# Kernel tuning notes

Hardware: AMD Instinct MI355X
Metric: run time of the kernel (lower is better)

Reference implementation:

```python
import jax, jax.numpy as jnp
import numpy as np

B, S, D, H, DH = 4, 1024, 1024, 16, 64  # batch, seq, d_model, heads, head dim (d_Q=d_K=d_V)


def setup_inputs() -> dict:
    key = jax.random.key(0)
    ks = jax.random.split(key, 12)
    std = 0.02
    return {
        "x_Q": jax.random.normal(ks[0], (B, S, D), jnp.float32),
        "x_K": jax.random.normal(ks[1], (B, S, D), jnp.float32),
        "x_V": jax.random.normal(ks[2], (B, S, D), jnp.float32),
        "src_batch_lens": jax.random.randint(ks[3], (B,), 0, S),
        # stacked per-head projection weights: [H, d_model, head_dim]
        "Wq": jax.random.normal(ks[4], (H, D, DH), jnp.float32) * std,
        "bq": jax.random.normal(ks[5], (H, DH), jnp.float32) * std,
        "Wk": jax.random.normal(ks[6], (H, D, DH), jnp.float32) * std,
        "bk": jax.random.normal(ks[7], (H, DH), jnp.float32) * std,
        "Wv": jax.random.normal(ks[8], (H, D, DH), jnp.float32) * std,
        "bv": jax.random.normal(ks[9], (H, DH), jnp.float32) * std,
        "Wo": jax.random.normal(ks[10], (D, D), jnp.float32) * std,
        "bo": jax.random.normal(ks[11], (D,), jnp.float32) * std,
    }


def reference(x_Q, x_K, x_V, src_batch_lens, Wq, bq, Wk, bk, Wv, bv, Wo, bo):
    dq = Wq.shape[-1]
    seq = x_Q.shape[1]
    # all heads at once instead of the per-head python loop
    Q = jnp.einsum('bsd,hde->bhse', x_Q, Wq) + bq[None, :, None, :]
    K = jnp.einsum('bsd,hde->bhse', x_K, Wk) + bk[None, :, None, :]
    V = jnp.einsum('bsd,hde->bhse', x_V, Wv) + bv[None, :, None, :]
    scores = jnp.einsum('bhse,bhte->bhst', Q, K) / jnp.sqrt(jnp.asarray(dq, x_Q.dtype))
    # original: matmul(diag(1..1,0..0), scores) zeroes query rows >= length
    rowmask = (jnp.arange(seq)[None, :] < src_batch_lens[:, None])  # [B, S]
    scores = scores * rowmask[:, None, :, None].astype(scores.dtype)
    A = jax.nn.softmax(scores, axis=-1)  # torch Softmax(dim=2) on [B,S,S] per head = key axis
    AV = jnp.einsum('bhst,bhtv->bhsv', A, V)
    out = AV.transpose(0, 2, 1, 3).reshape(x_Q.shape[0], seq, -1)  # concat heads on dim 2
    return out @ Wo + bo  # dropout p=0 -> identity
```

## Files before the change

### kernel.cpp

```cpp
#include <hip/hip_runtime.h>
#include <stdint.h>

typedef short v8s __attribute__((ext_vector_type(8)));
typedef short v4s __attribute__((ext_vector_type(4)));
typedef float v4f __attribute__((ext_vector_type(4)));

#define AS1 __attribute__((address_space(1)))
#define AS3 __attribute__((address_space(3)))

__device__ __forceinline__ void glds16(const void* g, void* l) {
  __builtin_amdgcn_global_load_lds((const AS1 void*)g, (AS3 void*)l, 16, 0, 0);
}

__device__ __forceinline__ short f2bf(float f) {
  uint32_t u = __float_as_uint(f);
  u += 0x7fffu + ((u >> 16) & 1u);
  return (short)(u >> 16);
}


__global__ __launch_bounds__(256) void cast3_f32_bf16(
    const float* __restrict__ a, const float* __restrict__ b, const float* __restrict__ c,
    short* __restrict__ oa, short* __restrict__ ob, short* __restrict__ oc, int n4) {
  const float* in = (blockIdx.z == 0) ? a : (blockIdx.z == 1) ? b : c;
  short* out      = (blockIdx.z == 0) ? oa : (blockIdx.z == 1) ? ob : oc;
  int i = blockIdx.x * 256 + threadIdx.x;
  if (i < n4) {
    float4 v = ((const float4*)in)[i];
    short4 o = { f2bf(v.x), f2bf(v.y), f2bf(v.z), f2bf(v.w) };
    ((short4*)out)[i] = o;
  }
}

__global__ __launch_bounds__(256) void transpose_w_all(
    const float* __restrict__ wq, const float* __restrict__ wk, const float* __restrict__ wv,
    const float* __restrict__ wo,
    short* __restrict__ oq, short* __restrict__ ok, short* __restrict__ ov,
    short* __restrict__ oo) {
  __shared__ float tile[64][65];
  const int z = blockIdx.z;
  const float* in;
  short* out;
  int C, R, rb, cb;
  if (z < 3) {
    const int slice = blockIdx.y;
    in  = ((z == 0) ? wq : (z == 1) ? wk : wv) + (size_t)slice * 65536;
    out = ((z == 0) ? oq : (z == 1) ? ok : ov) + (size_t)slice * 65536;
    C = 64; R = 1024; rb = blockIdx.x * 64; cb = 0;
  } else {
    in = wo; out = oo;
    C = 1024; R = 1024; rb = blockIdx.x * 64; cb = blockIdx.y * 64;
  }
  int t = threadIdx.x;
  int col = t & 63, r0 = t >> 6;
#pragma unroll
  for (int i = 0; i < 16; ++i) {
    int row = r0 + i * 4;
    tile[row][col] = in[(size_t)(rb + row) * C + cb + col];
  }
  __syncthreads();
#pragma unroll
  for (int i = 0; i < 16; ++i) {
    int orow = r0 + i * 4;
    out[(size_t)(cb + orow) * R + rb + col] = f2bf(tile[col][orow]);
  }
}

template <int MR>
__device__ __forceinline__ void gemm_core(const short* __restrict__ Ag,
                                          const short* __restrict__ Bg,
                                          short* As, short* Bs,
                                          v4f (&acc)[MR / 32][4]) {
  constexpr int MT = MR / 32;
  constexpr int ASZ = MR * 32;
  constexpr int BSZ = 128 * 32;
  const int tid  = threadIdx.x;
  const int lane = tid & 63;
  const int w    = tid >> 6;
  const int quad = lane >> 4;
  const int c15  = lane & 15;
  const int wr   = (w >> 1) * (MR / 2);
  const int wc   = (w & 1) * 64;

  const int r0 = tid >> 2, p0 = tid & 3;
  const short* a0 = Ag + (size_t)r0 * 1024 + p0 * 8;
  const short* a1 = a0 + 64 * 1024;
  const short* b0 = Bg + (size_t)r0 * 1024 + p0 * 8;
  const short* b1 = b0 + 64 * 1024;
  short* lA = As + tid * 8;
  short* lB = Bs + tid * 8;

  auto issue = [&](int t, int buf) {
    const int o = t * 32;
    glds16(a0 + o, lA + buf * ASZ);
    if constexpr (MR == 128) glds16(a1 + o, lA + buf * ASZ + 2048);
    glds16(b0 + o, lB + buf * BSZ);
    glds16(b1 + o, lB + buf * BSZ + 2048);
  };

  issue(0, 0);
  issue(1, 1);

  for (int kb = 0; kb < 32; ++kb) {
    if constexpr (MR == 128)
      asm volatile("s_waitcnt vmcnt(4)\n\ts_barrier" ::: "memory");
    else
      asm volatile("s_waitcnt vmcnt(3)\n\ts_barrier" ::: "memory");

    const int t2 = kb + 2;
    issue(t2 < 32 ? t2 : 31, t2 % 3);

    const short* Ab = As + (kb % 3) * ASZ;
    const short* Bb = Bs + (kb % 3) * BSZ;

    v8s a[MT], b[4];
#pragma unroll
    for (int mt = 0; mt < MT; ++mt)
      a[mt] = *(const v8s*)(Ab + (wr + mt * 16 + c15) * 32 + quad * 8);
#pragma unroll
    for (int nt = 0; nt < 4; ++nt)
      b[nt] = *(const v8s*)(Bb + (wc + nt * 16 + c15) * 32 + quad * 8);
#pragma unroll
    for (int mt = 0; mt < MT; ++mt)
#pragma unroll
      for (int nt = 0; nt < 4; ++nt)
        acc[mt][nt] = __builtin_amdgcn_mfma_f32_16x16x32_bf16(a[mt], b[nt], acc[mt][nt], 0, 0, 0);
  }
}

__global__ __launch_bounds__(256, 3) void proj_gemm(
    const short* __restrict__ xQ, const short* __restrict__ xK, const short* __restrict__ xV,
    const short* __restrict__ WqT, const short* __restrict__ WkT, const short* __restrict__ WvT,
    const float* __restrict__ bq, const float* __restrict__ bk, const float* __restrict__ bv,
    short* __restrict__ Qb, short* __restrict__ Kb, short* __restrict__ Vtb) {
  __shared__ short As[12288];
  __shared__ short Bs[12288];
  const int lin = blockIdx.x;
  const int z = lin >> 8;
  const int r = lin & 255;
  const int nb = ((r >> 3) & 7) * 128;
  const int mb = (((r & 7) << 2) + (r >> 6)) * 128;
  const short* A    = (z == 0) ? xQ  : (z == 1) ? xK  : xV;
  const short* Bt   = (z == 0) ? WqT : (z == 1) ? WkT : WvT;
  const float* bias = (z == 0) ? bq  : (z == 1) ? bk  : bv;
  short* outp       = (z == 0) ? Qb  : (z == 1) ? Kb  : Vtb;
  v4f acc[4][4] = {};
  gemm_core<128>(A + (size_t)mb * 1024, Bt + (size_t)nb * 1024, As, Bs, acc);

  const int lane = threadIdx.x & 63, w = threadIdx.x >> 6;
  const int quad = lane >> 4, c15 = lane & 15;
  const int wr = (w >> 1) * 64, wc = (w & 1) * 64;
  const bool vmode = (z == 2);
#pragma unroll
  for (int nt = 0; nt < 4; ++nt) {
    const int gn = nb + wc + nt * 16 + c15;
    const float bb = bias[gn];
    const int h = gn >> 6, e = gn & 63;
#pragma unroll
    for (int mt = 0; mt < 4; ++mt) {
      if (!vmode) {
#pragma unroll
        for (int rr = 0; rr < 4; ++rr) {
          const int gm = mb + wr + mt * 16 + quad * 4 + rr;
          const int bi = gm >> 10, s = gm & 1023;
          const size_t base = (size_t)(bi * 16 + h) * 65536;
          outp[base + (size_t)s * 64 + e] = f2bf(acc[mt][nt][rr] + bb);
        }
      } else {
        const int gm0 = mb + wr + mt * 16 + quad * 4;
        const int bi = gm0 >> 10, s0 = gm0 & 1023;
        const size_t base = (size_t)(bi * 16 + h) * 65536;
        short4 st = { f2bf(acc[mt][nt][0] + bb), f2bf(acc[mt][nt][1] + bb),
                      f2bf(acc[mt][nt][2] + bb), f2bf(acc[mt][nt][3] + bb) };
        *(short4*)&outp[base + (size_t)e * 1024 + s0] = st;
      }
    }
  }
}

__global__ __launch_bounds__(256, 3) void out_gemm(
    const short* __restrict__ AV, const short* __restrict__ WoT,
    const float* __restrict__ bo, float* __restrict__ outp) {
  __shared__ short As[6144];
  __shared__ short Bs[12288];
  const int lin = blockIdx.x;
  const int nb = ((lin >> 3) & 7) * 128;
  const int mb = (((lin & 7) << 3) + (lin >> 6)) * 64;
  v4f acc[2][4] = {};
  gemm_core<64>(AV + (size_t)mb * 1024, WoT + (size_t)nb * 1024, As, Bs, acc);
  const int lane = threadIdx.x & 63, w = threadIdx.x >> 6;
  const int quad = lane >> 4, c15 = lane & 15;
  const int wr = (w >> 1) * 32, wc = (w & 1) * 64;
#pragma unroll
  for (int nt = 0; nt < 4; ++nt) {
    const int gn = nb + wc + nt * 16 + c15;
    const float bb = bo[gn];
#pragma unroll
    for (int mt = 0; mt < 2; ++mt)
#pragma unroll
      for (int r = 0; r < 4; ++r) {
        const int gm = mb + wr + mt * 16 + quad * 4 + r;
        outp[(size_t)gm * 1024 + gn] = acc[mt][nt][r] + bb;
      }
  }
}

__global__ __launch_bounds__(256, 2) void attn_kernel(
    const short* __restrict__ Qb, const short* __restrict__ Kb,
    const short* __restrict__ Vtb, const int* __restrict__ lens,
    short* __restrict__ AVb) {
  __shared__ short Ks[2][4096];
  __shared__ short Vs[2][4096];
  const int tid = threadIdx.x, lane = tid & 63, w = tid >> 6;
  const int quad = lane >> 4, c15 = lane & 15;
  const int flat = blockIdx.x;
  const int bh = (flat & 7) + 8 * ((flat >> 3) & 7);
  const int qg = flat >> 6;
  const int b = bh >> 4, h = bh & 15;
  const short* Qp = Qb  + (size_t)bh * 65536;
  const short* Kp = Kb  + (size_t)bh * 65536;
  const short* Vp = Vtb + (size_t)bh * 65536;
  const int len = lens[b];
  const int row0 = qg * 128 + w * 32;

  v8s bq_[2][2];
#pragma unroll
  for (int mg = 0; mg < 2; ++mg)
#pragma unroll
    for (int kf = 0; kf < 2; ++kf)
      bq_[mg][kf] = *(const v8s*)(Qp + (size_t)(row0 + mg * 16 + c15) * 64 + kf * 32 + quad * 8);

  float scale[2];
#pragma unroll
  for (int mg = 0; mg < 2; ++mg)
    scale[mg] = (row0 + mg * 16 + c15 < len) ? 0.125f : 0.0f;

  float sm[2] = { 0.f, 0.f };
  v4f o[2][4] = {};

  const int srow = tid >> 3, spart = tid & 7;
  const int gpart = spart ^ (srow & 7);
  const int kgo0 = srow * 64 + gpart * 8, kgo1 = (srow + 32) * 64 + gpart * 8;
  const int vgo0 = srow * 1024 + gpart * 8, vgo1 = (srow + 32) * 1024 + gpart * 8;
  const int l0 = tid * 8, l1 = 2048 + tid * 8;

  const int c7 = c15 & 7;
  const int krow = c15 * 128;
  const int koff0 = krow + ((quad) ^ c7) * 16;
  const int koff1 = krow + ((4 + quad) ^ c7) * 16;
  const int q2 = quad >> 1, h8 = (quad & 1) * 8;
  int voff[4];
#pragma unroll
  for (int nt = 0; nt < 4; ++nt)
    voff[nt] = krow + ((2 * nt + q2) ^ c7) * 16 + h8;

  glds16(Kp + kgo0, (char*)Ks[0] + l0 * 2);
  glds16(Kp + kgo1, (char*)Ks[0] + l1 * 2);
  glds16(Vp + vgo0, (char*)Vs[0] + l0 * 2);
  glds16(Vp + vgo1, (char*)Vs[0] + l1 * 2);

  for (int kb = 0; kb < 16; ++kb) {
    const int cur = kb & 1, nxt = cur ^ 1;
    __syncthreads();

    if (kb < 15) {
      const short* kt = Kp + (size_t)(kb + 1) * 4096;
      const short* vt = Vp + (kb + 1) * 64;
      glds16(kt + kgo0, (char*)Ks[nxt] + l0 * 2);
      glds16(kt + kgo1, (char*)Ks[nxt] + l1 * 2);
      glds16(vt + vgo0, (char*)Vs[nxt] + l0 * 2);
      glds16(vt + vgo1, (char*)Vs[nxt] + l1 * 2);
    }

    v8s ak[4][2];
#pragma unroll
    for (int nt = 0; nt < 4; ++nt) {
      ak[nt][0] = *(const v8s*)((const char*)Ks[cur] + nt * 2048 + koff0);
      ak[nt][1] = *(const v8s*)((const char*)Ks[cur] + nt * 2048 + koff1);
    }
    v4s av[4][4];
#pragma unroll
    for (int t = 0; t < 4; ++t)
#pragma unroll
      for (int nt = 0; nt < 4; ++nt)
        av[t][nt] = *(const v4s*)((const char*)Vs[cur] + t * 2048 + voff[nt]);

    v4f sc[2][4];
#pragma unroll
    for (int mg = 0; mg < 2; ++mg)
#pragma unroll
      for (int nt = 0; nt < 4; ++nt) {
        v4f z = {};
#pragma unroll
        for (int kf = 0; kf < 2; ++kf)
          z = __builtin_amdgcn_mfma_f32_16x16x32_bf16(ak[nt][kf], bq_[mg][kf], z, 0, 0, 0);
        sc[mg][nt] = z;
      }

    v4s pb[2][4];
#pragma unroll
    for (int mg = 0; mg < 2; ++mg)
#pragma unroll
      for (int nt = 0; nt < 4; ++nt) {
        v4s pv;
#pragma unroll
        for (int r = 0; r < 4; ++r) {
          float p = __expf(sc[mg][nt][r] * scale[mg]);
          sm[mg] += p;
          pv[r] = f2bf(p);
        }
        pb[mg][nt] = pv;
      }

#pragma unroll
    for (int mg = 0; mg < 2; ++mg)
#pragma unroll
      for (int t = 0; t < 4; ++t)
#pragma unroll
        for (int nt = 0; nt < 4; ++nt)
          o[mg][t] = __builtin_amdgcn_mfma_f32_16x16x16bf16_1k(av[t][nt], pb[mg][nt], o[mg][t], 0, 0, 0);
  }

#pragma unroll
  for (int mg = 0; mg < 2; ++mg) {
    sm[mg] += __shfl_xor(sm[mg], 16);
    sm[mg] += __shfl_xor(sm[mg], 32);
  }

#pragma unroll
  for (int mg = 0; mg < 2; ++mg) {
    const float inv = 1.0f / sm[mg];
    const size_t rowbase = (size_t)(b * 1024 + row0 + mg * 16 + c15) * 1024 + h * 64;
#pragma unroll
    for (int t = 0; t < 4; ++t) {
      short4 st = { f2bf(o[mg][t][0] * inv), f2bf(o[mg][t][1] * inv),
                    f2bf(o[mg][t][2] * inv), f2bf(o[mg][t][3] * inv) };
      *(short4*)&AVb[rowbase + t * 16 + quad * 4] = st;
    }
  }
}

extern "C" void kernel_launch(void* const* d_in, const int* in_sizes, int n_in,
                              void* d_out, int out_size, void* d_ws, size_t ws_size,
                              hipStream_t stream) {
  const float* xQ = (const float*)d_in[0];
  const float* xK = (const float*)d_in[1];
  const float* xV = (const float*)d_in[2];
  const int* lens = (const int*)d_in[3];
  const float* Wq = (const float*)d_in[4];
  const float* bq = (const float*)d_in[5];
  const float* Wk = (const float*)d_in[6];
  const float* bk = (const float*)d_in[7];
  const float* Wv = (const float*)d_in[8];
  const float* bv = (const float*)d_in[9];
  const float* Wo = (const float*)d_in[10];
  const float* bo = (const float*)d_in[11];
  float* out = (float*)d_out;

  char* ws = (char*)d_ws;
  short* xQb = (short*)(ws + 0);
  short* xKb = (short*)(ws + 8388608);
  short* xVb = (short*)(ws + 16777216);
  short* WqT = (short*)(ws + 25165824);
  short* WkT = (short*)(ws + 27262976);
  short* WvT = (short*)(ws + 29360128);
  short* WoT = (short*)(ws + 31457280);
  short* Qb  = (short*)(ws + 33554432);
  short* Kb  = (short*)(ws + 41943040);
  short* Vtb = (short*)(ws + 50331648);
  short* AVb = (short*)(ws + 58720256);

  cast3_f32_bf16<<<dim3(4096, 1, 3), 256, 0, stream>>>(xQ, xK, xV, xQb, xKb, xVb, 1048576);
  transpose_w_all<<<dim3(16, 16, 4), 256, 0, stream>>>(Wq, Wk, Wv, Wo, WqT, WkT, WvT, WoT);
  proj_gemm<<<dim3(768), 256, 0, stream>>>(xQb, xKb, xVb, WqT, WkT, WvT,
                                           bq, bk, bv, Qb, Kb, Vtb);
  attn_kernel<<<dim3(512), 256, 0, stream>>>(Qb, Kb, Vtb, lens, AVb);
  out_gemm<<<dim3(512), 256, 0, stream>>>(AVb, WoT, bo, out);
}
```

Measured before the change: 204.9 us.

## Swizzle GEMM LDS tiles and split attention across 8 waves per block

The GEMM core now XOR-swizzles the 16-byte chunk position within each LDS row, on both the global-to-LDS writes and the fragment reads, to cut LDS bank conflicts. The attention kernel moves to 512 threads per block, with each wave handling 16 query rows instead of 32. Each thread then issues one K and one V async load per tile instead of two. The aim is fewer registers per wave and more waves in flight to hide latency, at the cost of less Q-tile reuse of each K/V fragment read from LDS per wave.

```diff
diff --git a/kernel.cpp b/kernel.cpp
--- a/kernel.cpp
+++ b/kernel.cpp
@@ -82,7 +82,8 @@
   const int wr   = (w >> 1) * (MR / 2);
   const int wc   = (w & 1) * 64;
 
-  const int r0 = tid >> 2, p0 = tid & 3;
+  const int r0 = tid >> 2;
+  const int p0 = (tid & 3) ^ ((r0 & 3) ^ ((r0 >> 2) & 3));
   const short* a0 = Ag + (size_t)r0 * 1024 + p0 * 8;
   const short* a1 = a0 + 64 * 1024;
   const short* b0 = Bg + (size_t)r0 * 1024 + p0 * 8;
@@ -101,6 +102,9 @@
   issue(0, 0);
   issue(1, 1);
 
+  const int xs = (c15 & 3) ^ ((c15 >> 2) & 3);
+  const int rdoff = ((quad ^ xs)) * 8;
+
   for (int kb = 0; kb < 32; ++kb) {
     if constexpr (MR == 128)
       asm volatile("s_waitcnt vmcnt(4)\n\ts_barrier" ::: "memory");
@@ -116,10 +120,10 @@
     v8s a[MT], b[4];
 #pragma unroll
     for (int mt = 0; mt < MT; ++mt)
-      a[mt] = *(const v8s*)(Ab + (wr + mt * 16 + c15) * 32 + quad * 8);
+      a[mt] = *(const v8s*)(Ab + (wr + mt * 16 + c15) * 32 + rdoff);
 #pragma unroll
     for (int nt = 0; nt < 4; ++nt)
-      b[nt] = *(const v8s*)(Bb + (wc + nt * 16 + c15) * 32 + quad * 8);
+      b[nt] = *(const v8s*)(Bb + (wc + nt * 16 + c15) * 32 + rdoff);
 #pragma unroll
     for (int mt = 0; mt < MT; ++mt)
 #pragma unroll
@@ -205,7 +209,7 @@
   }
 }
 
-__global__ __launch_bounds__(256, 2) void attn_kernel(
+__global__ __launch_bounds__(512, 4) void attn_kernel(
     const short* __restrict__ Qb, const short* __restrict__ Kb,
     const short* __restrict__ Vtb, const int* __restrict__ lens,
     short* __restrict__ AVb) {
@@ -221,28 +225,22 @@
   const short* Kp = Kb  + (size_t)bh * 65536;
   const short* Vp = Vtb + (size_t)bh * 65536;
   const int len = lens[b];
-  const int row0 = qg * 128 + w * 32;
-
-  v8s bq_[2][2];
-#pragma unroll
-  for (int mg = 0; mg < 2; ++mg)
-#pragma unroll
-    for (int kf = 0; kf < 2; ++kf)
-      bq_[mg][kf] = *(const v8s*)(Qp + (size_t)(row0 + mg * 16 + c15) * 64 + kf * 32 + quad * 8);
-
-  float scale[2];
-#pragma unroll
-  for (int mg = 0; mg < 2; ++mg)
-    scale[mg] = (row0 + mg * 16 + c15 < len) ? 0.125f : 0.0f;
-
-  float sm[2] = { 0.f, 0.f };
-  v4f o[2][4] = {};
+  const int row0 = qg * 128 + w * 16;
+
+  v8s bq_[2];
+#pragma unroll
+  for (int kf = 0; kf < 2; ++kf)
+    bq_[kf] = *(const v8s*)(Qp + (size_t)(row0 + c15) * 64 + kf * 32 + quad * 8);
+
+  const float scale = (row0 + c15 < len) ? 0.125f : 0.0f;
+  float sm = 0.f;
+  v4f o[4] = {};
 
   const int srow = tid >> 3, spart = tid & 7;
   const int gpart = spart ^ (srow & 7);
-  const int kgo0 = srow * 64 + gpart * 8, kgo1 = (srow + 32) * 64 + gpart * 8;
-  const int vgo0 = srow * 1024 + gpart * 8, vgo1 = (srow + 32) * 1024 + gpart * 8;
-  const int l0 = tid * 8, l1 = 2048 + tid * 8;
+  const int kgo = srow * 64 + gpart * 8;
+  const int vgo = srow * 1024 + gpart * 8;
+  const int l0 = tid * 8;
 
   const int c7 = c15 & 7;
   const int krow = c15 * 128;
@@ -254,22 +252,16 @@
   for (int nt = 0; nt < 4; ++nt)
     voff[nt] = krow + ((2 * nt + q2) ^ c7) * 16 + h8;
 
-  glds16(Kp + kgo0, (char*)Ks[0] + l0 * 2);
-  glds16(Kp + kgo1, (char*)Ks[0] + l1 * 2);
-  glds16(Vp + vgo0, (char*)Vs[0] + l0 * 2);
-  glds16(Vp + vgo1, (char*)Vs[0] + l1 * 2);
+  glds16(Kp + kgo, (char*)Ks[0] + l0 * 2);
+  glds16(Vp + vgo, (char*)Vs[0] + l0 * 2);
 
   for (int kb = 0; kb < 16; ++kb) {
     const int cur = kb & 1, nxt = cur ^ 1;
     __syncthreads();
 
     if (kb < 15) {
-      const short* kt = Kp + (size_t)(kb + 1) * 4096;
-      const short* vt = Vp + (kb + 1) * 64;
-      glds16(kt + kgo0, (char*)Ks[nxt] + l0 * 2);
-      glds16(kt + kgo1, (char*)Ks[nxt] + l1 * 2);
-      glds16(vt + vgo0, (char*)Vs[nxt] + l0 * 2);
-      glds16(vt + vgo1, (char*)Vs[nxt] + l1 * 2);
+      glds16(Kp + (size_t)(kb + 1) * 4096 + kgo, (char*)Ks[nxt] + l0 * 2);
+      glds16(Vp + (kb + 1) * 64 + vgo, (char*)Vs[nxt] + l0 * 2);
     }
 
     v8s ak[4][2];
@@ -278,6 +270,30 @@
       ak[nt][0] = *(const v8s*)((const char*)Ks[cur] + nt * 2048 + koff0);
       ak[nt][1] = *(const v8s*)((const char*)Ks[cur] + nt * 2048 + koff1);
     }
+
+    v4f sc[4];
+#pragma unroll
+    for (int nt = 0; nt < 4; ++nt) {
+      v4f z = {};
+#pragma unroll
+      for (int kf = 0; kf < 2; ++kf)
+        z = __builtin_amdgcn_mfma_f32_16x16x32_bf16(ak[nt][kf], bq_[kf], z, 0, 0, 0);
+      sc[nt] = z;
+    }
+
+    v4s pb[4];
+#pragma unroll
+    for (int nt = 0; nt < 4; ++nt) {
+      v4s pv;
+#pragma unroll
+      for (int r = 0; r < 4; ++r) {
+        float p = __expf(sc[nt][r] * scale);
+        sm += p;
+        pv[r] = f2bf(p);
+      }
+      pb[nt] = pv;
+    }
+
     v4s av[4][4];
 #pragma unroll
     for (int t = 0; t < 4; ++t)
@@ -285,58 +301,23 @@
       for (int nt = 0; nt < 4; ++nt)
         av[t][nt] = *(const v4s*)((const char*)Vs[cur] + t * 2048 + voff[nt]);
 
-    v4f sc[2][4];
-#pragma unroll
-    for (int mg = 0; mg < 2; ++mg)
-#pragma unroll
-      for (int nt = 0; nt < 4; ++nt) {
-        v4f z = {};
-#pragma unroll
-        for (int kf = 0; kf < 2; ++kf)
-          z = __builtin_amdgcn_mfma_f32_16x16x32_bf16(ak[nt][kf], bq_[mg][kf], z, 0, 0, 0);
-        sc[mg][nt] = z;
-      }
-
-    v4s pb[2][4];
-#pragma unroll
-    for (int mg = 0; mg < 2; ++mg)
-#pragma unroll
-      for (int nt = 0; nt < 4; ++nt) {
-        v4s pv;
-#pragma unroll
-        for (int r = 0; r < 4; ++r) {
-          float p = __expf(sc[mg][nt][r] * scale[mg]);
-          sm[mg] += p;
-          pv[r] = f2bf(p);
-        }
-        pb[mg][nt] = pv;
-      }
-
-#pragma unroll
-    for (int mg = 0; mg < 2; ++mg)
-#pragma unroll
-      for (int t = 0; t < 4; ++t)
-#pragma unroll
-        for (int nt = 0; nt < 4; ++nt)
-          o[mg][t] = __builtin_amdgcn_mfma_f32_16x16x16bf16_1k(av[t][nt], pb[mg][nt], o[mg][t], 0, 0, 0);
-  }
-
-#pragma unroll
-  for (int mg = 0; mg < 2; ++mg) {
-    sm[mg] += __shfl_xor(sm[mg], 16);
-    sm[mg] += __shfl_xor(sm[mg], 32);
-  }
-
-#pragma unroll
-  for (int mg = 0; mg < 2; ++mg) {
-    const float inv = 1.0f / sm[mg];
-    const size_t rowbase = (size_t)(b * 1024 + row0 + mg * 16 + c15) * 1024 + h * 64;
-#pragma unroll
-    for (int t = 0; t < 4; ++t) {
-      short4 st = { f2bf(o[mg][t][0] * inv), f2bf(o[mg][t][1] * inv),
-                    f2bf(o[mg][t][2] * inv), f2bf(o[mg][t][3] * inv) };
-      *(short4*)&AVb[rowbase + t * 16 + quad * 4] = st;
-    }
+#pragma unroll
+    for (int t = 0; t < 4; ++t)
+#pragma unroll
+      for (int nt = 0; nt < 4; ++nt)
+        o[t] = __builtin_amdgcn_mfma_f32_16x16x16bf16_1k(av[t][nt], pb[nt], o[t], 0, 0, 0);
+  }
+
+  sm += __shfl_xor(sm, 16);
+  sm += __shfl_xor(sm, 32);
+
+  const float inv = 1.0f / sm;
+  const size_t rowbase = (size_t)(b * 1024 + row0 + c15) * 1024 + h * 64;
+#pragma unroll
+  for (int t = 0; t < 4; ++t) {
+    short4 st = { f2bf(o[t][0] * inv), f2bf(o[t][1] * inv),
+                  f2bf(o[t][2] * inv), f2bf(o[t][3] * inv) };
+    *(short4*)&AVb[rowbase + t * 16 + quad * 4] = st;
   }
 }
 
@@ -374,6 +355,6 @@
   transpose_w_all<<<dim3(16, 16, 4), 256, 0, stream>>>(Wq, Wk, Wv, Wo, WqT, WkT, WvT, WoT);
   proj_gemm<<<dim3(768), 256, 0, stream>>>(xQb, xKb, xVb, WqT, WkT, WvT,
                                            bq, bk, bv, Qb, Kb, Vtb);
-  attn_kernel<<<dim3(512), 256, 0, stream>>>(Qb, Kb, Vtb, lens, AVb);
+  attn_kernel<<<dim3(512), 512, 0, stream>>>(Qb, Kb, Vtb, lens, AVb);
   out_gemm<<<dim3(512), 256, 0, stream>>>(AVb, WoT, bo, out);
 }
```

After: 205.2 us. About the same (+0.2%).
